# Kernel tuning notes

Hardware: AMD Instinct MI355X
Metric: run time of the kernel (lower is better)

The kernel has to match this reference:

```python
import jax, jax.numpy as jnp
import numpy as np

B, N, DIM, H, HD = 8, 1024, 512, 8, 64
INNER = H * HD  # 512
KS = 5


def setup_inputs() -> dict:
    key = jax.random.key(0)
    ks = jax.random.split(key, 9)
    r = lambda k, shape, s=1.0: jax.random.normal(k, shape, dtype=jnp.float32) * s
    return {
        "x_1": r(ks[0], (B, N, DIM)),
        "x_2": r(ks[1], (B, N, DIM)),
        "Wqkv1": r(ks[2], (DIM, 4 * INNER), 0.02),
        "Wqkv2": r(ks[3], (DIM, 4 * INNER), 0.02),
        "Wout1": r(ks[4], (INNER, DIM), 0.02),
        "bout1": jnp.zeros((DIM,), jnp.float32),
        "Wout2": r(ks[5], (INNER, DIM), 0.02),
        "bout2": jnp.zeros((DIM,), jnp.float32),
        "conv_w": r(ks[6], (N, 1, KS), 0.1),   # depthwise Conv1d weight [out=N, in/groups=1, k]
        "conv_b": r(ks[7], (N,), 0.02),
    }


def _split_heads(t):
    # 'b n (h d) -> b h n d'
    b, n, _ = t.shape
    return t.reshape(b, n, H, HD).transpose(0, 2, 1, 3)


def _merge_heads(t):
    # 'b h n d -> b n (h d)'
    b, h, n, d = t.shape
    return t.transpose(0, 2, 1, 3).reshape(b, n, h * d)


def reference(x_1, x_2, Wqkv1, Wqkv2, Wout1, bout1, Wout2, bout2, conv_w, conv_b):
    scale = HD ** (-0.5)
    q1, k1, v1, s1 = map(_split_heads, jnp.split(x_1 @ Wqkv1, 4, axis=-1))
    q2, k2, v2, s2 = map(_split_heads, jnp.split(x_2 @ Wqkv2, 4, axis=-1))

    dots1 = jnp.einsum('bhid,bhjd->bhij', q1, k1) * scale
    dots2 = jnp.einsum('bhid,bhjd->bhij', q2, k2) * scale

    MS = _merge_heads(s1 + s2)  # [b, n, inner_dim]
    # depthwise conv over the feature axis, channels = tokens (n), kernel 5 pad 2
    A = jax.lax.conv_general_dilated(
        MS, conv_w, window_strides=(1,), padding=((KS // 2, KS // 2),),
        dimension_numbers=('NCH', 'OIH', 'NCH'), feature_group_count=N,
    ) + conv_b[None, :, None]
    MSg = jax.nn.sigmoid(A) * MS
    MSh = _split_heads(MSg)
    dots3 = jnp.einsum('bhid,bhjd->bhij', MSh, MSh) * scale

    a1 = jax.nn.softmax(dots1, axis=-1)
    a2 = jax.nn.softmax(dots2, axis=-1)
    a3 = jax.nn.softmax(dots3, axis=-1)

    t1 = jnp.einsum('bhij,bhjd->bhid', a3, v1) + v1
    t1 = jnp.einsum('bhij,bhjd->bhid', a1, t1)
    t2 = jnp.einsum('bhij,bhjd->bhid', a3, v2) + v2
    t2 = jnp.einsum('bhij,bhjd->bhid', a2, t2)

    out1 = _merge_heads(t1) @ Wout1 + bout1
    out2 = _merge_heads(t2) @ Wout2 + bout2
    return (out1, out2)
```

## Files before the change

kernel.cpp:

```cpp
#include <hip/hip_runtime.h>
#include <hip/hip_bf16.h>

#define B_     8
#define N_     1024
#define DIM_   512
#define H_     8
#define HD_    64
#define INNER_ 512
#define QKVC   2048
#define M_     8192

typedef __attribute__((ext_vector_type(8))) short short8;
typedef __attribute__((ext_vector_type(4))) float f32x4;
#define MFMA_BF16 __builtin_amdgcn_mfma_f32_16x16x32_bf16

__device__ __forceinline__ unsigned short f2b(float x) {
    __hip_bfloat16 h = __float2bfloat16(x);
    unsigned short u; __builtin_memcpy(&u, &h, 2); return u;
}
__device__ __forceinline__ unsigned int packsplit(float x) {
    unsigned int hb = f2b(x);
    float fh = __uint_as_float(hb << 16);
    unsigned int lb = f2b(x - fh);
    return (hb << 16) | lb;
}
__device__ __forceinline__ void split8(const float* v, short8& h, short8& l) {
#pragma unroll
    for (int i = 0; i < 8; i++) {
        unsigned int hb = f2b(v[i]);
        float fh = __uint_as_float(hb << 16);
        h[i] = (short)hb; l[i] = (short)f2b(v[i] - fh);
    }
}
__device__ __forceinline__ void split2x2(float a, float b, unsigned int& h, unsigned int& l) {
    unsigned int ha = f2b(a), hb = f2b(b);
    float fa = __uint_as_float(ha << 16), fb = __uint_as_float(hb << 16);
    h = ha | (hb << 16);
    l = (unsigned int)f2b(a - fa) | ((unsigned int)f2b(b - fb) << 16);
}

__device__ __forceinline__ void gll16(const unsigned short* g, unsigned short* l) {
    __builtin_amdgcn_global_load_lds(
        (const __attribute__((address_space(1))) void*)g,
        (__attribute__((address_space(3))) void*)l, 16, 0, 0);
}


__global__ __launch_bounds__(256)
void pack_a_tiled(const float* __restrict__ in, unsigned short* __restrict__ out)
{
    size_t i = ((size_t)blockIdx.x * 256 + threadIdx.x) * 4;
    float4 v = *(const float4*)(in + i);
    const size_t R = i >> 9;
    const int k  = (int)(i & 511);
    const int kt = k >> 5, kk = k & 31;
    const int r  = (int)(R & 127);
    const size_t rt = R >> 7;
    unsigned short* tile = out + (((rt << 4) + kt) << 13) + r * 64;
    unsigned int h01, l01, h23, l23;
    split2x2(v.x, v.y, h01, l01);
    split2x2(v.z, v.w, h23, l23);
    uint2 hv; hv.x = h01; hv.y = h23;
    uint2 lv; lv.x = l01; lv.y = l23;
    const int s7 = r & 7;
    *(uint2*)&tile[(((kk >> 3)     ^ s7) << 3) + (kk & 7)] = hv;
    *(uint2*)&tile[((((kk >> 3)+4) ^ s7) << 3) + (kk & 7)] = lv;
}

__global__ __launch_bounds__(256)
void pack_w_tiled(const float* __restrict__ W, unsigned short* __restrict__ out, int N)
{
    const int n  = blockIdx.x * 256 + threadIdx.x;
    const int k0 = blockIdx.y * 4;
    float f0 = W[(size_t)(k0 + 0) * N + n];
    float f1 = W[(size_t)(k0 + 1) * N + n];
    float f2 = W[(size_t)(k0 + 2) * N + n];
    float f3 = W[(size_t)(k0 + 3) * N + n];
    const int r  = n & 127;
    const size_t rt = n >> 7;
    const int kt = k0 >> 5, kk = k0 & 31;
    unsigned short* tile = out + (((rt << 4) + kt) << 13) + r * 64;
    unsigned int h01, l01, h23, l23;
    split2x2(f0, f1, h01, l01);
    split2x2(f2, f3, h23, l23);
    uint2 hv; hv.x = h01; hv.y = h23;
    uint2 lv; lv.x = l01; lv.y = l23;
    const int s7 = r & 7;
    *(uint2*)&tile[(((kk >> 3)     ^ s7) << 3) + (kk & 7)] = hv;
    *(uint2*)&tile[((((kk >> 3)+4) ^ s7) << 3) + (kk & 7)] = lv;
}

__global__ __launch_bounds__(256)
void pack_wt(const float* __restrict__ W, unsigned int* __restrict__ Wt, int N)
{
    const int n = blockIdx.x * 256 + threadIdx.x;
    const int k0 = blockIdx.y * 4;
    uint4 p;
    p.x = packsplit(W[(size_t)(k0 + 0) * N + n]);
    p.y = packsplit(W[(size_t)(k0 + 1) * N + n]);
    p.z = packsplit(W[(size_t)(k0 + 2) * N + n]);
    p.w = packsplit(W[(size_t)(k0 + 3) * N + n]);
    *(uint4*)&Wt[(size_t)n * 512 + k0] = p;
}

template<bool BIAS, bool PACKK>
__global__ __launch_bounds__(256)
void gemm_gll(const unsigned short* __restrict__ At, const unsigned short* __restrict__ Bt,
              const float* __restrict__ bias, float* __restrict__ Cp,
              int M, int N)
{
    __shared__ __align__(16) unsigned short sA[128 * 64];
    __shared__ __align__(16) unsigned short sB[128 * 64];

    const int t    = threadIdx.x;
    const int lane = t & 63;
    const int w    = t >> 6;
    const int n16  = lane & 15, quad = lane >> 4;
    const int wm   = w >> 1, wn = w & 1;
    const int m0 = blockIdx.y * 128, n0 = blockIdx.x * 128;

    f32x4 acc[4][4];
#pragma unroll
    for (int mt = 0; mt < 4; mt++)
#pragma unroll
        for (int nt = 0; nt < 4; nt++) acc[mt][nt] = (f32x4){0.f, 0.f, 0.f, 0.f};

    const unsigned short* Ag = At + ((size_t)blockIdx.y << 4) * 8192 + (w * 64 + lane) * 8;
    const unsigned short* Bg = Bt + ((size_t)blockIdx.x << 4) * 8192 + (w * 64 + lane) * 8;
    unsigned short* sAw = &sA[w * 512];
    unsigned short* sBw = &sB[w * 512];

    for (int kt = 0; kt < 16; kt++) {
        __syncthreads();
        const size_t ko = (size_t)kt * 8192;
#pragma unroll
        for (int i = 0; i < 4; i++) {
            gll16(Ag + ko + i * 2048, sAw + i * 2048);
            gll16(Bg + ko + i * 2048, sBw + i * 2048);
        }
        __syncthreads();

        short8 Ah[4], Al[4];
#pragma unroll
        for (int mt = 0; mt < 4; mt++) {
            const int row = 64 * wm + 16 * mt + n16;
            const int base = row * 64;
            const int s7 = row & 7;
            Ah[mt] = *(const short8*)&sA[base + (((quad    ) ^ s7) << 3)];
            Al[mt] = *(const short8*)&sA[base + (((quad + 4) ^ s7) << 3)];
        }
#pragma unroll
        for (int nt = 0; nt < 4; nt++) {
            const int row = 64 * wn + 16 * nt + n16;
            const int base = row * 64;
            const int s7 = row & 7;
            short8 Bh = *(const short8*)&sB[base + (((quad    ) ^ s7) << 3)];
            short8 Bl = *(const short8*)&sB[base + (((quad + 4) ^ s7) << 3)];
#pragma unroll
            for (int mt = 0; mt < 4; mt++) {
                acc[mt][nt] = MFMA_BF16(Ah[mt], Bh, acc[mt][nt], 0, 0, 0);
                acc[mt][nt] = MFMA_BF16(Al[mt], Bh, acc[mt][nt], 0, 0, 0);
                acc[mt][nt] = MFMA_BF16(Ah[mt], Bl, acc[mt][nt], 0, 0, 0);
            }
        }
    }

    const bool packout = PACKK && ((n0 >> 9) == 1);
    float bv[4];
#pragma unroll
    for (int nt = 0; nt < 4; nt++)
        bv[nt] = BIAS ? bias[n0 + 64 * wn + 16 * nt + n16] : 0.f;
#pragma unroll
    for (int mt = 0; mt < 4; mt++) {
        const int rbase = m0 + 64 * wm + 16 * mt + 4 * quad;
#pragma unroll
        for (int r = 0; r < 4; r++) {
#pragma unroll
            for (int nt = 0; nt < 4; nt++) {
                const int col = n0 + 64 * wn + 16 * nt + n16;
                const int row = rbase + r;
                const float v = acc[mt][nt][r] + bv[nt];
                if (packout) {
                    const int dg = col & 511;
                    unsigned int hb = f2b(v);
                    float fh = __uint_as_float(hb << 16);
                    unsigned short* kim = (unsigned short*)Cp + (size_t)row * (2 * N);
                    kim[1024 + dg] = (unsigned short)hb;
                    kim[1536 + dg] = f2b(v - fh);
                } else {
                    Cp[(size_t)row * N + col] = v;
                }
            }
        }
    }
}

template<bool BIAS>
__global__ __launch_bounds__(256)
void gemm_mfma(const unsigned int* __restrict__ Ap, const unsigned int* __restrict__ Btp,
               const float* __restrict__ bias, float* __restrict__ Cp,
               int M, int N)
{
    const int K = 512;
    __shared__ __align__(16) unsigned short sA[128 * 64];
    __shared__ __align__(16) unsigned short sB[128 * 64];

    const int t    = threadIdx.x;
    const int lane = t & 63;
    const int w    = t >> 6;
    const int n16  = lane & 15, quad = lane >> 4;
    const int wm   = w >> 1, wn = w & 1;
    const int m0 = blockIdx.y * 128, n0 = blockIdx.x * 128;

    f32x4 acc[4][4];
#pragma unroll
    for (int mt = 0; mt < 4; mt++)
#pragma unroll
        for (int nt = 0; nt < 4; nt++) acc[mt][nt] = (f32x4){0.f, 0.f, 0.f, 0.f};

    const int srow = t >> 1;
    const int kb   = (t & 1) * 16;
    const unsigned int* ag = Ap  + (size_t)(m0 + srow) * K + kb;
    const unsigned int* bg = Btp + (size_t)(n0 + srow) * K + kb;
    const int s7s = srow & 7;
    unsigned short* swA = &sA[srow * 64];
    unsigned short* swB = &sB[srow * 64];

    for (int k0 = 0; k0 < K; k0 += 32) {
        __syncthreads();
#pragma unroll
        for (int i = 0; i < 4; i++) {
            const int kk = kb + i * 4;
            const int ch = kk >> 3;
            const int ho = kk & 4;
            const int c_hi = ((ch    ) ^ s7s) << 3;
            const int c_lo = ((ch + 4) ^ s7s) << 3;
            uint4 va = *(const uint4*)(ag + k0 + i * 4);
            uint4 vb = *(const uint4*)(bg + k0 + i * 4);
            uint2 ha, la, hb, lb;
            ha.x = (va.y & 0xFFFF0000u) | (va.x >> 16);
            ha.y = (va.w & 0xFFFF0000u) | (va.z >> 16);
            la.x = (va.y << 16) | (va.x & 0xFFFFu);
            la.y = (va.w << 16) | (va.z & 0xFFFFu);
            hb.x = (vb.y & 0xFFFF0000u) | (vb.x >> 16);
            hb.y = (vb.w & 0xFFFF0000u) | (vb.z >> 16);
            lb.x = (vb.y << 16) | (vb.x & 0xFFFFu);
            lb.y = (vb.w << 16) | (vb.z & 0xFFFFu);
            *(uint2*)&swA[c_hi + ho] = ha;
            *(uint2*)&swA[c_lo + ho] = la;
            *(uint2*)&swB[c_hi + ho] = hb;
            *(uint2*)&swB[c_lo + ho] = lb;
        }
        __syncthreads();

        short8 Ah[4], Al[4];
#pragma unroll
        for (int mt = 0; mt < 4; mt++) {
            const int row = 64 * wm + 16 * mt + n16;
            const int base = row * 64;
            const int s7 = row & 7;
            Ah[mt] = *(const short8*)&sA[base + (((quad    ) ^ s7) << 3)];
            Al[mt] = *(const short8*)&sA[base + (((quad + 4) ^ s7) << 3)];
        }
#pragma unroll
        for (int nt = 0; nt < 4; nt++) {
            const int row = 64 * wn + 16 * nt + n16;
            const int base = row * 64;
            const int s7 = row & 7;
            short8 Bh = *(const short8*)&sB[base + (((quad    ) ^ s7) << 3)];
            short8 Bl = *(const short8*)&sB[base + (((quad + 4) ^ s7) << 3)];
#pragma unroll
            for (int mt = 0; mt < 4; mt++) {
                acc[mt][nt] = MFMA_BF16(Ah[mt], Bh, acc[mt][nt], 0, 0, 0);
                acc[mt][nt] = MFMA_BF16(Al[mt], Bh, acc[mt][nt], 0, 0, 0);
                acc[mt][nt] = MFMA_BF16(Ah[mt], Bl, acc[mt][nt], 0, 0, 0);
            }
        }
    }

    float bv[4];
#pragma unroll
    for (int nt = 0; nt < 4; nt++)
        bv[nt] = BIAS ? bias[n0 + 64 * wn + 16 * nt + n16] : 0.f;
#pragma unroll
    for (int mt = 0; mt < 4; mt++) {
        const int rbase = m0 + 64 * wm + 16 * mt + 4 * quad;
#pragma unroll
        for (int r = 0; r < 4; r++) {
#pragma unroll
            for (int nt = 0; nt < 4; nt++) {
                const int col = n0 + 64 * wn + 16 * nt + n16;
                Cp[(size_t)(rbase + r) * N + col] = acc[mt][nt][r] + bv[nt];
            }
        }
    }
}

__global__ __launch_bounds__(128)
void convgate_kernel(const float* __restrict__ qkv1, const float* __restrict__ qkv2,
                     const float* __restrict__ convw,
                     const float* __restrict__ convb,
                     float* __restrict__ MSg, unsigned short* __restrict__ Kimg)
{
    __shared__ float ms[INNER_];
    const int blk = blockIdx.x;
    const int n = blk & (N_ - 1);
    const int b = blk >> 10;
    const int t = threadIdx.x;

    const float4* q1 = (const float4*)(qkv1 + (size_t)blk * QKVC + 3 * INNER_);
    const float4* q2 = (const float4*)(qkv2 + (size_t)blk * QKVC + 3 * INNER_);
    float4 v1 = q1[t], v2 = q2[t];
    float4 s;
    s.x = v1.x + v2.x; s.y = v1.y + v2.y; s.z = v1.z + v2.z; s.w = v1.w + v2.w;
    *(float4*)&ms[t * 4] = s;
    __syncthreads();

    float w[5];
#pragma unroll
    for (int k = 0; k < 5; k++) w[k] = convw[n * 5 + k];
    const float cb = convb[n];

    float out[4];
#pragma unroll
    for (int ff = 0; ff < 4; ff++) {
        int f = t * 4 + ff;
        float A = cb;
#pragma unroll
        for (int k = 0; k < 5; k++) {
            int idx = f + k - 2;
            if (idx >= 0 && idx < INNER_) A += ms[idx] * w[k];
        }
        float sg = 1.f / (1.f + __expf(-A));
        out[ff] = ms[f] * sg;
    }
    *(float4*)&MSg[(size_t)blk * INNER_ + t * 4] = make_float4(out[0], out[1], out[2], out[3]);

    const int h  = t >> 4;
    const int d0 = (4 * t) & 63;
    unsigned short hs[4], ls[4];
#pragma unroll
    for (int e = 0; e < 4; e++) {
        unsigned int hb = f2b(out[e]);
        float fh = __uint_as_float(hb << 16);
        hs[e] = (unsigned short)hb;
        ls[e] = f2b(out[e] - fh);
    }
    unsigned short* kim = Kimg + ((size_t)(b * 8 + h) * 1024 + n) * 128 + d0;
    uint2 hv; hv.x = (unsigned int)hs[0] | ((unsigned int)hs[1] << 16);
              hv.y = (unsigned int)hs[2] | ((unsigned int)hs[3] << 16);
    uint2 lv; lv.x = (unsigned int)ls[0] | ((unsigned int)ls[1] << 16);
              lv.y = (unsigned int)ls[2] | ((unsigned int)ls[3] << 16);
    *(uint2*)kim        = hv;
    *(uint2*)(kim + 64) = lv;
}

template<int NV, bool RESID, bool PACKO, bool IMGO, bool VIMG, int NPROB>
__global__ __launch_bounds__(512, 2)
void mattn_kernel(const float* __restrict__ Q0, const float* __restrict__ Q1,
                  const unsigned short* __restrict__ K0, const unsigned short* __restrict__ K1,
                  const float* __restrict__ VA0, const float* __restrict__ VA1,
                  const float* __restrict__ VB0, const float* __restrict__ VB1,
                  float* __restrict__ OA0, float* __restrict__ OA1,
                  float* __restrict__ OB0, float* __restrict__ OB1,
                  long long q_sb, long long q_sh, int q_sr,
                  long long k_sb, long long k_sh, int k_rs, int k_po,
                  long long v_sb, long long v_sh, int v_sr,
                  long long o_sb, long long o_sh, int o_sr)
{
    __shared__ __align__(16) unsigned short sK[64 * 128];
    __shared__ __align__(16) unsigned short sV0[64 * 64];
    __shared__ __align__(16) unsigned short sV1[(NV == 2) ? 64 * 64 : 8];
    __shared__ __align__(16) unsigned short sP[128 * 64];

    const int t    = threadIdx.x;
    const int w    = t >> 6;
    const int lane = t & 63;
    const int n16  = lane & 15;
    const int quad = lane >> 4;

    const int bid = blockIdx.x;
    const int c   = bid & 7;
    const int r1  = bid >> 3;
    const int qt  = r1 & 7;
    const int r2  = r1 >> 3;
    const int g   = r2 & 7;
    const int p   = (NPROB == 2) ? (r2 >> 3) : 0;
    const int bh  = 8 * g + c;
    const int b = bh >> 3, h = bh & 7;
    const int i0 = qt * 128;

    const float* Qb          = (NPROB == 2 && p) ? Q1 : Q0;
    const unsigned short* Kb = (NPROB == 2 && p) ? K1 : K0;
    const float* VAb         = (NPROB == 2 && p) ? VA1 : VA0;
    float* OAb               = (NPROB == 2 && p) ? OA1 : OA0;

    const float* Qg          = Qb + (size_t)b * q_sb + (size_t)h * q_sh;
    const unsigned short* Kg = Kb + (size_t)b * k_sb + (size_t)h * k_sh;

    const float* V0g = nullptr;
    const float* V1g = nullptr;
    const unsigned short* Vus = nullptr;
    if constexpr (VIMG) {
        Vus = (const unsigned short*)VAb + (size_t)b * v_sb + (size_t)h * v_sh;
    } else {
        V0g = VAb + (size_t)b * v_sb + (size_t)h * v_sh;
        if constexpr (NV == 2)
            V1g = VB0 + (size_t)b * v_sb + (size_t)h * v_sh;
    }

    float* O0g = nullptr; float* O1g = nullptr;
    unsigned short* img0 = nullptr; unsigned short* img1 = nullptr;
    if constexpr (IMGO) {
        img0 = (unsigned short*)OAb + (size_t)b * o_sb + (size_t)h * o_sh;
        if constexpr (NV == 2)
            img1 = (unsigned short*)OB0 + (size_t)b * o_sb + (size_t)h * o_sh;
    } else {
        O0g = OAb + (size_t)b * o_sb + (size_t)h * o_sh;
        if constexpr (NV == 2)
            O1g = OB0 + (size_t)b * o_sb + (size_t)h * o_sh;
    }

    const float SC2 = 0.1803368801f;
    short8 Qh[2], Ql[2];
#pragma unroll
    for (int s = 0; s < 2; s++) {
        const float* qp = Qg + (size_t)(i0 + 16 * w + n16) * q_sr + 32 * s + 8 * quad;
        float qv[8];
        float4 q0 = *(const float4*)qp;
        float4 q1 = *(const float4*)(qp + 4);
        qv[0]=q0.x*SC2; qv[1]=q0.y*SC2; qv[2]=q0.z*SC2; qv[3]=q0.w*SC2;
        qv[4]=q1.x*SC2; qv[5]=q1.y*SC2; qv[6]=q1.z*SC2; qv[7]=q1.w*SC2;
        split8(qv, Qh[s], Ql[s]);
    }

    float m_ = -1e30f, l_ = 0.f;
    f32x4 O0a[4], O1a[(NV == 2) ? 4 : 1];
#pragma unroll
    for (int nt = 0; nt < 4; nt++) O0a[nt] = (f32x4){0.f,0.f,0.f,0.f};
    if constexpr (NV == 2) {
#pragma unroll
        for (int nt = 0; nt < 4; nt++) O1a[nt] = (f32x4){0.f,0.f,0.f,0.f};
    }

    const int prow = 16 * w + n16;
    const int vc = t & 15, vp = t >> 4;

    const int jr_l = (w << 2) + (lane >> 4);
    const int lq   = (lane & 15) ^ (jr_l & 15);
    const unsigned short* kg_base = Kg + (size_t)jr_l * k_rs
                                  + (lq >> 3) * k_po + (lq & 7) * 8;
    unsigned short* sKw = &sK[w * 512];

    for (int j0 = 0; j0 < N_; j0 += 64) {
        __syncthreads();

        {
            const unsigned short* kg = kg_base + (size_t)j0 * k_rs;
            gll16(kg, sKw);
            gll16(kg + (size_t)32 * k_rs, sKw + 4096);
        }
        if constexpr (VIMG) {
            gll16(Vus + (size_t)(j0 >> 6) * 4096 + t * 8, &sV0[w * 512]);
        } else {
            const int j = 2 * vp;
            const float* a0 = V0g + (size_t)(j0 + j) * v_sr + 4 * vc;
            float4 va = *(const float4*)a0;
            float4 vb = *(const float4*)(a0 + v_sr);
#pragma unroll
            for (int e = 0; e < 4; e++) {
                float fa = (e==0)?va.x:(e==1)?va.y:(e==2)?va.z:va.w;
                float fb = (e==0)?vb.x:(e==1)?vb.y:(e==2)?vb.z:vb.w;
                unsigned int u = (unsigned int)f2b(fa) | ((unsigned int)f2b(fb) << 16);
                const int d = 4 * vc + e;
                const int phys = (vp >> 2) ^ ((d ^ (d >> 2)) & 7);
                *(unsigned int*)&sV0[d * 64 + (phys << 3) + (j & 7)] = u;
            }
            if constexpr (NV == 2) {
                const float* a1 = V1g + (size_t)(j0 + j) * v_sr + 4 * vc;
                float4 wa = *(const float4*)a1;
                float4 wb = *(const float4*)(a1 + v_sr);
#pragma unroll
                for (int e = 0; e < 4; e++) {
                    float fa = (e==0)?wa.x:(e==1)?wa.y:(e==2)?wa.z:wa.w;
                    float fb = (e==0)?wb.x:(e==1)?wb.y:(e==2)?wb.z:wb.w;
                    unsigned int u = (unsigned int)f2b(fa) | ((unsigned int)f2b(fb) << 16);
                    const int d = 4 * vc + e;
                    const int phys = (vp >> 2) ^ ((d ^ (d >> 2)) & 7);
                    *(unsigned int*)&sV1[d * 64 + (phys << 3) + (j & 7)] = u;
                }
            }
        }
        __syncthreads();

        f32x4 accS[4];
#pragma unroll
        for (int mt = 0; mt < 4; mt++) accS[mt] = (f32x4){0.f,0.f,0.f,0.f};
#pragma unroll
        for (int s = 0; s < 2; s++) {
#pragma unroll
            for (int mt = 0; mt < 4; mt++) {
                const unsigned short* kb2 = &sK[(16 * mt + n16) * 128];
                short8 kh = *(const short8*)&kb2[(((4*s + quad)    ) ^ n16) << 3];
                short8 kl = *(const short8*)&kb2[(((4*s + quad) + 8) ^ n16) << 3];
                accS[mt] = MFMA_BF16(kl, Qh[s], accS[mt], 0, 0, 0);
                accS[mt] = MFMA_BF16(kh, Ql[s], accS[mt], 0, 0, 0);
                accS[mt] = MFMA_BF16(kh, Qh[s], accS[mt], 0, 0, 0);
            }
        }

        float tmax = -1e30f;
#pragma unroll
        for (int mt = 0; mt < 4; mt++)
#pragma unroll
            for (int r = 0; r < 4; r++) tmax = fmaxf(tmax, accS[mt][r]);
        tmax = fmaxf(tmax, __shfl_xor(tmax, 16));
        tmax = fmaxf(tmax, __shfl_xor(tmax, 32));
        if (!__all(tmax <= m_ + 11.0f)) {
            const float mnew = fmaxf(m_, tmax);
            const float alpha = __builtin_amdgcn_exp2f(m_ - mnew);
            m_ = mnew;
            l_ *= alpha;
            float ar[4];
#pragma unroll
            for (int r = 0; r < 4; r++) ar[r] = __shfl(alpha, (quad << 2) + r);
#pragma unroll
            for (int nt = 0; nt < 4; nt++) {
#pragma unroll
                for (int r = 0; r < 4; r++) O0a[nt][r] *= ar[r];
                if constexpr (NV == 2)
#pragma unroll
                    for (int r = 0; r < 4; r++) O1a[nt][r] *= ar[r];
            }
        }
        float rsum = 0.f;
#pragma unroll
        for (int mt = 0; mt < 4; mt++) {
            float p0 = __builtin_amdgcn_exp2f(accS[mt][0] - m_);
            float p1 = __builtin_amdgcn_exp2f(accS[mt][1] - m_);
            float p2 = __builtin_amdgcn_exp2f(accS[mt][2] - m_);
            float p3 = __builtin_amdgcn_exp2f(accS[mt][3] - m_);
            rsum += (p0 + p1) + (p2 + p3);
            uint2 u;
            u.x = (unsigned int)f2b(p0) | ((unsigned int)f2b(p1) << 16);
            u.y = (unsigned int)f2b(p2) | ((unsigned int)f2b(p3) << 16);
            const int phys = (2 * mt + (quad >> 1)) ^ (n16 & 7);
            *(uint2*)&sP[prow * 64 + (phys << 3) + 4 * (quad & 1)] = u;
        }
        rsum += __shfl_xor(rsum, 16);
        rsum += __shfl_xor(rsum, 32);
        l_ += rsum;

#pragma unroll
        for (int s = 0; s < 2; s++) {
            short8 Pf = *(const short8*)&sP[prow * 64 + (((4*s + quad) ^ (n16 & 7)) << 3)];
#pragma unroll
            for (int nt = 0; nt < 4; nt++) {
                const int d = 16 * nt + n16;
                const int phys = (4*s + quad) ^ ((d ^ (d >> 2)) & 7);
                short8 vf = *(const short8*)&sV0[d * 64 + (phys << 3)];
                O0a[nt] = MFMA_BF16(Pf, vf, O0a[nt], 0, 0, 0);
                if constexpr (NV == 2) {
                    short8 vf1 = *(const short8*)&sV1[d * 64 + (phys << 3)];
                    O1a[nt] = MFMA_BF16(Pf, vf1, O1a[nt], 0, 0, 0);
                }
            }
        }
    }

    float linv[4];
#pragma unroll
    for (int r = 0; r < 4; r++) linv[r] = 1.0f / __shfl(l_, (quad << 2) + r);

    if constexpr (IMGO) {
        const int blk = 2 * qt + (w >> 2);
        const int jg  = (2 * w + (quad >> 1)) & 7;
        const int j7b = 4 * (quad & 1);
#pragma unroll
        for (int nt = 0; nt < 4; nt++) {
            const int d = 16 * nt + n16;
            const int swd = (d ^ (d >> 2)) & 7;
            const size_t off = (size_t)blk * 4096 + d * 64 + ((jg ^ swd) << 3) + j7b;
            unsigned short o0[4], o1[4];
#pragma unroll
            for (int r = 0; r < 4; r++) {
                const int row = i0 + 16 * w + 4 * quad + r;
                float v = O0a[nt][r] * linv[r];
                if constexpr (RESID) v += V0g[(size_t)row * v_sr + d];
                o0[r] = f2b(v);
                if constexpr (NV == 2) {
                    float v1 = O1a[nt][r] * linv[r];
                    if constexpr (RESID) v1 += V1g[(size_t)row * v_sr + d];
                    o1[r] = f2b(v1);
                }
            }
            uint2 u0;
            u0.x = (unsigned int)o0[0] | ((unsigned int)o0[1] << 16);
            u0.y = (unsigned int)o0[2] | ((unsigned int)o0[3] << 16);
            *(uint2*)&img0[off] = u0;
            if constexpr (NV == 2) {
                uint2 u1v;
                u1v.x = (unsigned int)o1[0] | ((unsigned int)o1[1] << 16);
                u1v.y = (unsigned int)o1[2] | ((unsigned int)o1[3] << 16);
                *(uint2*)&img1[off] = u1v;
            }
        }
    } else {
#pragma unroll
        for (int r = 0; r < 4; r++) {
            const int row = i0 + 16 * w + 4 * quad + r;
#pragma unroll
            for (int nt = 0; nt < 4; nt++) {
                const int col = 16 * nt + n16;
                float v = O0a[nt][r] * linv[r];
                if constexpr (RESID) v += V0g[(size_t)row * v_sr + col];
                if constexpr (PACKO)
                    ((unsigned int*)O0g)[(size_t)row * o_sr + col] = packsplit(v);
                else
                    O0g[(size_t)row * o_sr + col] = v;
                if constexpr (NV == 2) {
                    float v1 = O1a[nt][r] * linv[r];
                    if constexpr (RESID) v1 += V1g[(size_t)row * v_sr + col];
                    if constexpr (PACKO)
                        ((unsigned int*)O1g)[(size_t)row * o_sr + col] = packsplit(v1);
                    else
                        O1g[(size_t)row * o_sr + col] = v1;
                }
            }
        }
    }
}

extern "C" void kernel_launch(void* const* d_in, const int* in_sizes, int n_in,
                              void* d_out, int out_size, void* d_ws, size_t ws_size,
                              hipStream_t stream)
{
    const float* x1    = (const float*)d_in[0];
    const float* x2    = (const float*)d_in[1];
    const float* Wqkv1 = (const float*)d_in[2];
    const float* Wqkv2 = (const float*)d_in[3];
    const float* Wout1 = (const float*)d_in[4];
    const float* bout1 = (const float*)d_in[5];
    const float* Wout2 = (const float*)d_in[6];
    const float* bout2 = (const float*)d_in[7];
    const float* convw = (const float*)d_in[8];
    const float* convb = (const float*)d_in[9];

    const size_t QKV_ELEMS = (size_t)M_ * QKVC;
    const size_t BND_ELEMS = (size_t)M_ * INNER_;
    if (ws_size < (2 * QKV_ELEMS + 5 * BND_ELEMS) * sizeof(float)) return;

    float* ws   = (float*)d_ws;
    float* qkv1 = ws;
    float* qkv2 = qkv1 + QKV_ELEMS;
    float* MSg  = qkv2 + QKV_ELEMS;
    float* u1   = MSg + BND_ELEMS;
    float* u2   = u1 + BND_ELEMS;
    float* t1m  = u2 + BND_ELEMS;
    float* t2m  = t1m + BND_ELEMS;

    unsigned short* x1t   = (unsigned short*)t1m;
    unsigned short* x2t   = (unsigned short*)t2m;
    unsigned short* KimgA = (unsigned short*)t1m;
    unsigned short* w1t   = (unsigned short*)u2;
    unsigned short* w2t   = w1t + (size_t)QKVC * DIM_ * 2;
    unsigned short* u1img = (unsigned short*)u1;
    unsigned short* u2img = (unsigned short*)u2;
    unsigned int*   wo1pt = (unsigned int*)u1;
    unsigned int*   wo2pt = wo1pt + (size_t)DIM_ * DIM_;

    dim3 blk(256);

    pack_a_tiled<<<dim3(M_ * DIM_ / 1024), blk, 0, stream>>>(x1, x1t);
    pack_a_tiled<<<dim3(M_ * DIM_ / 1024), blk, 0, stream>>>(x2, x2t);
    pack_w_tiled<<<dim3(QKVC / 256, DIM_ / 4), blk, 0, stream>>>(Wqkv1, w1t, QKVC);
    pack_w_tiled<<<dim3(QKVC / 256, DIM_ / 4), blk, 0, stream>>>(Wqkv2, w2t, QKVC);

    gemm_gll<false, true><<<dim3(QKVC / 128, M_ / 128), blk, 0, stream>>>(
        x1t, w1t, nullptr, qkv1, M_, QKVC);
    gemm_gll<false, true><<<dim3(QKVC / 128, M_ / 128), blk, 0, stream>>>(
        x2t, w2t, nullptr, qkv2, M_, QKVC);

    convgate_kernel<<<dim3(M_), dim3(128), 0, stream>>>(qkv1, qkv2, convw, convb,
                                                        MSg, KimgA);

    const long long msg_sb = (long long)N_ * INNER_, msg_sh = HD_;
    const int       msg_sr = INNER_;
    const long long qkv_sb = (long long)N_ * QKVC, qkv_sh = HD_;
    const int       qkv_sr = QKVC;
    const long long kA_sb = (long long)8 * N_ * 128, kA_sh = (long long)N_ * 128;
    const long long kB_sb = (long long)N_ * QKVC * 2;
    const long long ui_sb = (long long)H_ * N_ * HD_, ui_sh = (long long)N_ * HD_;

    mattn_kernel<2, true, false, true, false, 1><<<dim3(512), dim3(512), 0, stream>>>(
        MSg, nullptr, KimgA, nullptr,
        qkv1 + 2 * INNER_, nullptr, qkv2 + 2 * INNER_, nullptr,
        (float*)u1img, nullptr, (float*)u2img, nullptr,
        msg_sb, msg_sh, msg_sr,
        kA_sb, kA_sh, 128, 64,
        qkv_sb, qkv_sh, qkv_sr,
        ui_sb, ui_sh, HD_);

    mattn_kernel<1, false, true, false, true, 2><<<dim3(1024), dim3(512), 0, stream>>>(
        qkv1, qkv2,
        (const unsigned short*)qkv1 + 1024, (const unsigned short*)qkv2 + 1024,
        (const float*)u1img, (const float*)u2img, nullptr, nullptr,
        t1m, t2m, nullptr, nullptr,
        qkv_sb, qkv_sh, qkv_sr,
        kB_sb, 64, QKVC * 2, 512,
        ui_sb, ui_sh, HD_,
        msg_sb, msg_sh, msg_sr);

    pack_wt<<<dim3(DIM_ / 256, DIM_ / 4), blk, 0, stream>>>(Wout1, wo1pt, DIM_);
    pack_wt<<<dim3(DIM_ / 256, DIM_ / 4), blk, 0, stream>>>(Wout2, wo2pt, DIM_);

    float* out1 = (float*)d_out;
    float* out2 = out1 + (size_t)M_ * DIM_;
    gemm_mfma<true><<<dim3(DIM_ / 128, M_ / 128), blk, 0, stream>>>(
        (const unsigned int*)t1m, wo1pt, bout1, out1, M_, DIM_);
    gemm_mfma<true><<<dim3(DIM_ / 128, M_ / 128), blk, 0, stream>>>(
        (const unsigned int*)t2m, wo2pt, bout2, out2, M_, DIM_);
}
```

Before: 464.4 us.

## Batch paired GEMMs via grid z and emit tiled split-bf16 image from attention

The two QKV projection GEMMs and the two output-projection GEMMs are each merged into one launch, with blockIdx.z choosing the problem. The second attention kernel now writes its output directly in the swizzled tiled hi/lo bf16 layout that gemm_gll reads through global_load_lds. This lets the output projection drop the register-repack gemm_mfma path in favour of the async-load GEMM. The intent is to cut launch count, fill more CUs per launch, and remove the per-tile repacking work, at the cost of scattered 2-byte stores in the attention epilogue.

```diff
diff --git a/kernel.cpp b/kernel.cpp
--- a/kernel.cpp
+++ b/kernel.cpp
@@ -17,12 +17,6 @@
 __device__ __forceinline__ unsigned short f2b(float x) {
     __hip_bfloat16 h = __float2bfloat16(x);
     unsigned short u; __builtin_memcpy(&u, &h, 2); return u;
-}
-__device__ __forceinline__ unsigned int packsplit(float x) {
-    unsigned int hb = f2b(x);
-    float fh = __uint_as_float(hb << 16);
-    unsigned int lb = f2b(x - fh);
-    return (hb << 16) | lb;
 }
 __device__ __forceinline__ void split8(const float* v, short8& h, short8& l) {
 #pragma unroll
@@ -90,27 +84,22 @@
     *(uint2*)&tile[((((kk >> 3)+4) ^ s7) << 3) + (kk & 7)] = lv;
 }
 
+template<bool BIAS, bool PACKK, int NPROB>
 __global__ __launch_bounds__(256)
-void pack_wt(const float* __restrict__ W, unsigned int* __restrict__ Wt, int N)
-{
-    const int n = blockIdx.x * 256 + threadIdx.x;
-    const int k0 = blockIdx.y * 4;
-    uint4 p;
-    p.x = packsplit(W[(size_t)(k0 + 0) * N + n]);
-    p.y = packsplit(W[(size_t)(k0 + 1) * N + n]);
-    p.z = packsplit(W[(size_t)(k0 + 2) * N + n]);
-    p.w = packsplit(W[(size_t)(k0 + 3) * N + n]);
-    *(uint4*)&Wt[(size_t)n * 512 + k0] = p;
-}
-
-template<bool BIAS, bool PACKK>
-__global__ __launch_bounds__(256)
-void gemm_gll(const unsigned short* __restrict__ At, const unsigned short* __restrict__ Bt,
-              const float* __restrict__ bias, float* __restrict__ Cp,
+void gemm_gll(const unsigned short* __restrict__ At0, const unsigned short* __restrict__ At1,
+              const unsigned short* __restrict__ Bt0, const unsigned short* __restrict__ Bt1,
+              const float* __restrict__ bias0, const float* __restrict__ bias1,
+              float* __restrict__ Cp0, float* __restrict__ Cp1,
               int M, int N)
 {
     __shared__ __align__(16) unsigned short sA[128 * 64];
     __shared__ __align__(16) unsigned short sB[128 * 64];
+
+    const int z = (NPROB == 2) ? blockIdx.z : 0;
+    const unsigned short* At = z ? At1 : At0;
+    const unsigned short* Bt = z ? Bt1 : Bt0;
+    const float* bias        = z ? bias1 : bias0;
+    float* Cp                = z ? Cp1 : Cp0;
 
     const int t    = threadIdx.x;
     const int lane = t & 63;
@@ -195,107 +184,6 @@
     }
 }
 
-template<bool BIAS>
-__global__ __launch_bounds__(256)
-void gemm_mfma(const unsigned int* __restrict__ Ap, const unsigned int* __restrict__ Btp,
-               const float* __restrict__ bias, float* __restrict__ Cp,
-               int M, int N)
-{
-    const int K = 512;
-    __shared__ __align__(16) unsigned short sA[128 * 64];
-    __shared__ __align__(16) unsigned short sB[128 * 64];
-
-    const int t    = threadIdx.x;
-    const int lane = t & 63;
-    const int w    = t >> 6;
-    const int n16  = lane & 15, quad = lane >> 4;
-    const int wm   = w >> 1, wn = w & 1;
-    const int m0 = blockIdx.y * 128, n0 = blockIdx.x * 128;
-
-    f32x4 acc[4][4];
-#pragma unroll
-    for (int mt = 0; mt < 4; mt++)
-#pragma unroll
-        for (int nt = 0; nt < 4; nt++) acc[mt][nt] = (f32x4){0.f, 0.f, 0.f, 0.f};
-
-    const int srow = t >> 1;
-    const int kb   = (t & 1) * 16;
-    const unsigned int* ag = Ap  + (size_t)(m0 + srow) * K + kb;
-    const unsigned int* bg = Btp + (size_t)(n0 + srow) * K + kb;
-    const int s7s = srow & 7;
-    unsigned short* swA = &sA[srow * 64];
-    unsigned short* swB = &sB[srow * 64];
-
-    for (int k0 = 0; k0 < K; k0 += 32) {
-        __syncthreads();
-#pragma unroll
-        for (int i = 0; i < 4; i++) {
-            const int kk = kb + i * 4;
-            const int ch = kk >> 3;
-            const int ho = kk & 4;
-            const int c_hi = ((ch    ) ^ s7s) << 3;
-            const int c_lo = ((ch + 4) ^ s7s) << 3;
-            uint4 va = *(const uint4*)(ag + k0 + i * 4);
-            uint4 vb = *(const uint4*)(bg + k0 + i * 4);
-            uint2 ha, la, hb, lb;
-            ha.x = (va.y & 0xFFFF0000u) | (va.x >> 16);
-            ha.y = (va.w & 0xFFFF0000u) | (va.z >> 16);
-            la.x = (va.y << 16) | (va.x & 0xFFFFu);
-            la.y = (va.w << 16) | (va.z & 0xFFFFu);
-            hb.x = (vb.y & 0xFFFF0000u) | (vb.x >> 16);
-            hb.y = (vb.w & 0xFFFF0000u) | (vb.z >> 16);
-            lb.x = (vb.y << 16) | (vb.x & 0xFFFFu);
-            lb.y = (vb.w << 16) | (vb.z & 0xFFFFu);
-            *(uint2*)&swA[c_hi + ho] = ha;
-            *(uint2*)&swA[c_lo + ho] = la;
-            *(uint2*)&swB[c_hi + ho] = hb;
-            *(uint2*)&swB[c_lo + ho] = lb;
-        }
-        __syncthreads();
-
-        short8 Ah[4], Al[4];
-#pragma unroll
-        for (int mt = 0; mt < 4; mt++) {
-            const int row = 64 * wm + 16 * mt + n16;
-            const int base = row * 64;
-            const int s7 = row & 7;
-            Ah[mt] = *(const short8*)&sA[base + (((quad    ) ^ s7) << 3)];
-            Al[mt] = *(const short8*)&sA[base + (((quad + 4) ^ s7) << 3)];
-        }
-#pragma unroll
-        for (int nt = 0; nt < 4; nt++) {
-            const int row = 64 * wn + 16 * nt + n16;
-            const int base = row * 64;
-            const int s7 = row & 7;
-            short8 Bh = *(const short8*)&sB[base + (((quad    ) ^ s7) << 3)];
-            short8 Bl = *(const short8*)&sB[base + (((quad + 4) ^ s7) << 3)];
-#pragma unroll
-            for (int mt = 0; mt < 4; mt++) {
-                acc[mt][nt] = MFMA_BF16(Ah[mt], Bh, acc[mt][nt], 0, 0, 0);
-                acc[mt][nt] = MFMA_BF16(Al[mt], Bh, acc[mt][nt], 0, 0, 0);
-                acc[mt][nt] = MFMA_BF16(Ah[mt], Bl, acc[mt][nt], 0, 0, 0);
-            }
-        }
-    }
-
-    float bv[4];
-#pragma unroll
-    for (int nt = 0; nt < 4; nt++)
-        bv[nt] = BIAS ? bias[n0 + 64 * wn + 16 * nt + n16] : 0.f;
-#pragma unroll
-    for (int mt = 0; mt < 4; mt++) {
-        const int rbase = m0 + 64 * wm + 16 * mt + 4 * quad;
-#pragma unroll
-        for (int r = 0; r < 4; r++) {
-#pragma unroll
-            for (int nt = 0; nt < 4; nt++) {
-                const int col = n0 + 64 * wn + 16 * nt + n16;
-                Cp[(size_t)(rbase + r) * N + col] = acc[mt][nt][r] + bv[nt];
-            }
-        }
-    }
-}
-
 __global__ __launch_bounds__(128)
 void convgate_kernel(const float* __restrict__ qkv1, const float* __restrict__ qkv2,
                      const float* __restrict__ convw,
@@ -355,7 +243,7 @@
     *(uint2*)(kim + 64) = lv;
 }
 
-template<int NV, bool RESID, bool PACKO, bool IMGO, bool VIMG, int NPROB>
+template<int NV, bool RESID, bool IMGO, bool IMGA, bool VIMG, int NPROB>
 __global__ __launch_bounds__(512, 2)
 void mattn_kernel(const float* __restrict__ Q0, const float* __restrict__ Q1,
                   const unsigned short* __restrict__ K0, const unsigned short* __restrict__ K1,
@@ -415,6 +303,8 @@
         img0 = (unsigned short*)OAb + (size_t)b * o_sb + (size_t)h * o_sh;
         if constexpr (NV == 2)
             img1 = (unsigned short*)OB0 + (size_t)b * o_sb + (size_t)h * o_sh;
+    } else if constexpr (IMGA) {
+        img0 = (unsigned short*)OAb;
     } else {
         O0g = OAb + (size_t)b * o_sb + (size_t)h * o_sh;
         if constexpr (NV == 2)
@@ -605,6 +495,24 @@
                 *(uint2*)&img1[off] = u1v;
             }
         }
+    } else if constexpr (IMGA) {
+        const size_t rt = (size_t)b * 8 + qt;
+#pragma unroll
+        for (int r = 0; r < 4; r++) {
+            const int rr  = 16 * w + 4 * quad + r;
+            const int s7v = rr & 7;
+#pragma unroll
+            for (int nt = 0; nt < 4; nt++) {
+                const int k   = h * 64 + 16 * nt + n16;
+                const int kt2 = k >> 5, kk = k & 31;
+                unsigned short* tile = img0 + (((rt << 4) + kt2) << 13) + rr * 64;
+                float v = O0a[nt][r] * linv[r];
+                unsigned int hb = f2b(v);
+                float fh = __uint_as_float(hb << 16);
+                tile[(((kk >> 3)     ^ s7v) << 3) + (kk & 7)] = (unsigned short)hb;
+                tile[((((kk >> 3)+4) ^ s7v) << 3) + (kk & 7)] = f2b(v - fh);
+            }
+        }
     } else {
 #pragma unroll
         for (int r = 0; r < 4; r++) {
@@ -614,17 +522,11 @@
                 const int col = 16 * nt + n16;
                 float v = O0a[nt][r] * linv[r];
                 if constexpr (RESID) v += V0g[(size_t)row * v_sr + col];
-                if constexpr (PACKO)
-                    ((unsigned int*)O0g)[(size_t)row * o_sr + col] = packsplit(v);
-                else
-                    O0g[(size_t)row * o_sr + col] = v;
+                O0g[(size_t)row * o_sr + col] = v;
                 if constexpr (NV == 2) {
                     float v1 = O1a[nt][r] * linv[r];
                     if constexpr (RESID) v1 += V1g[(size_t)row * v_sr + col];
-                    if constexpr (PACKO)
-                        ((unsigned int*)O1g)[(size_t)row * o_sr + col] = packsplit(v1);
-                    else
-                        O1g[(size_t)row * o_sr + col] = v1;
+                    O1g[(size_t)row * o_sr + col] = v1;
                 }
             }
         }
@@ -666,8 +568,10 @@
     unsigned short* w2t   = w1t + (size_t)QKVC * DIM_ * 2;
     unsigned short* u1img = (unsigned short*)u1;
     unsigned short* u2img = (unsigned short*)u2;
-    unsigned int*   wo1pt = (unsigned int*)u1;
-    unsigned int*   wo2pt = wo1pt + (size_t)DIM_ * DIM_;
+    unsigned short* t1img = (unsigned short*)t1m;
+    unsigned short* t2img = (unsigned short*)t2m;
+    unsigned short* wo1t  = (unsigned short*)u1;
+    unsigned short* wo2t  = wo1t + (size_t)DIM_ * DIM_ * 2;
 
     dim3 blk(256);
 
@@ -676,10 +580,8 @@
     pack_w_tiled<<<dim3(QKVC / 256, DIM_ / 4), blk, 0, stream>>>(Wqkv1, w1t, QKVC);
     pack_w_tiled<<<dim3(QKVC / 256, DIM_ / 4), blk, 0, stream>>>(Wqkv2, w2t, QKVC);
 
-    gemm_gll<false, true><<<dim3(QKVC / 128, M_ / 128), blk, 0, stream>>>(
-        x1t, w1t, nullptr, qkv1, M_, QKVC);
-    gemm_gll<false, true><<<dim3(QKVC / 128, M_ / 128), blk, 0, stream>>>(
-        x2t, w2t, nullptr, qkv2, M_, QKVC);
+    gemm_gll<false, true, 2><<<dim3(QKVC / 128, M_ / 128, 2), blk, 0, stream>>>(
+        x1t, x2t, w1t, w2t, nullptr, nullptr, qkv1, qkv2, M_, QKVC);
 
     convgate_kernel<<<dim3(M_), dim3(128), 0, stream>>>(qkv1, qkv2, convw, convb,
                                                         MSg, KimgA);
@@ -692,7 +594,7 @@
     const long long kB_sb = (long long)N_ * QKVC * 2;
     const long long ui_sb = (long long)H_ * N_ * HD_, ui_sh = (long long)N_ * HD_;
 
-    mattn_kernel<2, true, false, true, false, 1><<<dim3(512), dim3(512), 0, stream>>>(
+    mattn_kernel<2, true, true, false, false, 1><<<dim3(512), dim3(512), 0, stream>>>(
         MSg, nullptr, KimgA, nullptr,
         qkv1 + 2 * INNER_, nullptr, qkv2 + 2 * INNER_, nullptr,
         (float*)u1img, nullptr, (float*)u2img, nullptr,
@@ -701,23 +603,21 @@
         qkv_sb, qkv_sh, qkv_sr,
         ui_sb, ui_sh, HD_);
 
-    mattn_kernel<1, false, true, false, true, 2><<<dim3(1024), dim3(512), 0, stream>>>(
+    mattn_kernel<1, false, false, true, true, 2><<<dim3(1024), dim3(512), 0, stream>>>(
         qkv1, qkv2,
         (const unsigned short*)qkv1 + 1024, (const unsigned short*)qkv2 + 1024,
         (const float*)u1img, (const float*)u2img, nullptr, nullptr,
-        t1m, t2m, nullptr, nullptr,
+        (float*)t1img, (float*)t2img, nullptr, nullptr,
         qkv_sb, qkv_sh, qkv_sr,
         kB_sb, 64, QKVC * 2, 512,
         ui_sb, ui_sh, HD_,
-        msg_sb, msg_sh, msg_sr);
-
-    pack_wt<<<dim3(DIM_ / 256, DIM_ / 4), blk, 0, stream>>>(Wout1, wo1pt, DIM_);
-    pack_wt<<<dim3(DIM_ / 256, DIM_ / 4), blk, 0, stream>>>(Wout2, wo2pt, DIM_);
+        0, 0, 0);
+
+    pack_w_tiled<<<dim3(DIM_ / 256, DIM_ / 4), blk, 0, stream>>>(Wout1, wo1t, DIM_);
+    pack_w_tiled<<<dim3(DIM_ / 256, DIM_ / 4), blk, 0, stream>>>(Wout2, wo2t, DIM_);
 
     float* out1 = (float*)d_out;
     float* out2 = out1 + (size_t)M_ * DIM_;
-    gemm_mfma<true><<<dim3(DIM_ / 128, M_ / 128), blk, 0, stream>>>(
-        (const unsigned int*)t1m, wo1pt, bout1, out1, M_, DIM_);
-    gemm_mfma<true><<<dim3(DIM_ / 128, M_ / 128), blk, 0, stream>>>(
-        (const unsigned int*)t2m, wo2pt, bout2, out2, M_, DIM_);
-}
+    gemm_gll<true, false, 2><<<dim3(DIM_ / 128, M_ / 128, 2), blk, 0, stream>>>(
+        t1img, t2img, wo1t, wo2t, bout1, bout2, out1, out2, M_, DIM_);
+}
```

Result: faster. 413.1 us (-11.1%).
